# Kernel tuning notes

Hardware: AMD Instinct MI355X
Metric: run time of the kernel (lower is better)

The kernel has to match this reference:

```python
import jax, jax.numpy as jnp
import numpy as np

N_NODES = 50000
N_EDGES = 400000
HEADS = 4
OUT_CH = 128
IN_CH = 128
NEG_SLOPE = 0.2  # PyG GATConv default


def setup_inputs() -> dict:
    key = jax.random.key(0)
    ks = jax.random.split(key, 6)
    x = jax.random.normal(ks[0], (N_NODES, IN_CH), dtype=jnp.float32)
    edge_index = jax.random.randint(ks[1], (2, N_EDGES), 0, N_NODES, dtype=jnp.int64)
    # glorot-ish scaling for numerical sanity
    W = jax.random.normal(ks[2], (IN_CH, HEADS * OUT_CH), dtype=jnp.float32) * (1.0 / np.sqrt(IN_CH))
    att_src = jax.random.normal(ks[3], (1, HEADS, OUT_CH), dtype=jnp.float32) * (1.0 / np.sqrt(OUT_CH))
    att_dst = jax.random.normal(ks[4], (1, HEADS, OUT_CH), dtype=jnp.float32) * (1.0 / np.sqrt(OUT_CH))
    bias = jax.random.normal(ks[5], (HEADS * OUT_CH,), dtype=jnp.float32) * 0.01
    return {"x": x, "edge_index": edge_index, "W": W, "att_src": att_src, "att_dst": att_dst, "bias": bias}


def reference(x, edge_index, W, att_src, att_dst, bias):
    # PyG GATConv forward (eval mode -> attention dropout is identity), concat=True.
    N = x.shape[0]
    # add self loops (PyG default add_self_loops=True)
    loops = jnp.arange(N, dtype=edge_index.dtype)
    src = jnp.concatenate([edge_index[0], loops])  # message sources
    dst = jnp.concatenate([edge_index[1], loops])  # aggregation targets

    h = (x @ W).reshape(N, HEADS, OUT_CH)                 # [N,H,C]
    a_src = jnp.sum(h * att_src, axis=-1)                 # [N,H]
    a_dst = jnp.sum(h * att_dst, axis=-1)                 # [N,H]

    e = jax.nn.leaky_relu(a_src[src] + a_dst[dst], NEG_SLOPE)  # [E,H]
    # scatter-softmax over incoming edges of each dst node (every node has a self loop)
    e_max = jax.ops.segment_max(e, dst, num_segments=N)        # [N,H]
    e_exp = jnp.exp(e - e_max[dst])                            # [E,H]
    denom = jax.ops.segment_sum(e_exp, dst, num_segments=N)    # [N,H]
    alpha = e_exp / denom[dst]                                 # [E,H]

    msg = h[src] * alpha[:, :, None]                           # [E,H,C]
    out = jax.ops.segment_sum(msg, dst, num_segments=N)        # [N,H,C]
    return out.reshape(N, HEADS * OUT_CH) + bias
```

## Files before the change

### kernel.cpp

```cpp
#include <hip/hip_runtime.h>
#include <math.h>

#define N_NODES 50000
#define N_EDGES 400000
#define HEADS 4
#define CH 128
#define HC 512
#define NEG_SLOPE 0.2f
#define CAP 48

typedef float f32x4 __attribute__((ext_vector_type(4)));
typedef short bf16x8 __attribute__((ext_vector_type(8)));
typedef int   i32x4 __attribute__((ext_vector_type(4)));
typedef unsigned short u16x8 __attribute__((ext_vector_type(8)));

__device__ inline unsigned short f2bf(float f) {
    unsigned int u = __float_as_uint(f);
    unsigned int r = (u + 0x7FFFu + ((u >> 16) & 1u)) >> 16;
    return (unsigned short)r;
}
__device__ inline float bf2f(unsigned short u) {
    return __uint_as_float(((unsigned int)u) << 16);
}

#define CASTNB 256
#define ZNB    ((N_NODES + 255) / 256)
#define DEGNB  ((N_EDGES + 255) / 256)

__global__ __launch_bounds__(256) void k_prep(const float* __restrict__ W,
                                              unsigned short* __restrict__ Wsw,
                                              int* __restrict__ cnt) {
    const int bid = blockIdx.x, tid = threadIdx.x;
    if (bid < CASTNB) {
        int i = bid * 256 + tid;
        int k = i >> 9, n = i & 511;
        int kt = k >> 5, kk = k & 31;
        int nt = n >> 4, nn = n & 15;
        int lane = ((kk >> 3) << 4) | nn;
        int j = kk & 7;
        Wsw[((size_t)(kt * 32 + nt) * 64 + lane) * 8 + j] = f2bf(W[i]);
    } else {
        int i = (bid - CASTNB) * 256 + tid;
        if (i < N_NODES) cnt[i] = 0;
    }
}

__global__ __launch_bounds__(256) void k_fillslot(const int* __restrict__ ei,
                                                  int* __restrict__ cnt,
                                                  int* __restrict__ slot) {
    int e = blockIdx.x * 256 + threadIdx.x;
    if (e >= N_EDGES) return;
    int s = ei[e];
    int d = ei[N_EDGES + e];
    int pos = atomicAdd(&cnt[d], 1);
    if (pos < CAP) slot[d * CAP + pos] = s;
}

#define AP 136
#define OP 520
#define BM 16
#define GEMMNB (N_NODES / BM)

__global__ __launch_bounds__(256) void k_gemm(const float* __restrict__ x,
                                              const unsigned short* __restrict__ Wsw,
                                              const float* __restrict__ att_src,
                                              const float* __restrict__ att_dst,
                                              unsigned short* __restrict__ h,
                                              float* __restrict__ a_src,
                                              float* __restrict__ a_dst) {
    __shared__ unsigned short lds[BM * OP];

    const int r0  = blockIdx.x * BM;
    const int tid = threadIdx.x;

    {
        const f32x4* x4 = (const f32x4*)x;
#pragma unroll
        for (int i = 0; i < 2; ++i) {
            int idx = i * 256 + tid;
            int row = idx >> 5;
            int c4  = idx & 31;
            f32x4 v = __builtin_nontemporal_load(&x4[(size_t)(r0 + row) * 32 + c4]);
            ushort4 b;
            b.x = f2bf(v.x); b.y = f2bf(v.y); b.z = f2bf(v.z); b.w = f2bf(v.w);
            *(ushort4*)&lds[row * AP + c4 * 4] = b;
        }
    }
    __syncthreads();

    const int wave = tid >> 6;
    const int lane = tid & 63;
    const int mrow = lane & 15;
    const int kgrp = lane >> 4;
    const int ntg0 = wave * 8;

    f32x4 acc[8];
#pragma unroll
    for (int nt = 0; nt < 8; ++nt) acc[nt] = (f32x4)(0.f);

#pragma unroll
    for (int kt = 0; kt < 4; ++kt) {
        bf16x8 a0 = *(const bf16x8*)&lds[mrow * AP + kt * 32 + kgrp * 8];
#pragma unroll
        for (int nt = 0; nt < 8; ++nt) {
            bf16x8 b = *(const bf16x8*)&Wsw[((size_t)(kt * 32 + ntg0 + nt) * 64 + lane) * 8];
            acc[nt] = __builtin_amdgcn_mfma_f32_16x16x32_bf16(a0, b, acc[nt], 0, 0, 0);
        }
    }

    {
        float as[8], adv[8];
#pragma unroll
        for (int nt = 0; nt < 8; ++nt) {
            as[nt]  = att_src[wave * 128 + nt * 16 + mrow];
            adv[nt] = att_dst[wave * 128 + nt * 16 + mrow];
        }
#pragma unroll
        for (int r = 0; r < 4; ++r) {
            float sv = 0.f, dv = 0.f;
#pragma unroll
            for (int nt = 0; nt < 8; ++nt) {
                sv += acc[nt][r] * as[nt];
                dv += acc[nt][r] * adv[nt];
            }
#pragma unroll
            for (int off = 1; off < 16; off <<= 1) {
                sv += __shfl_xor(sv, off);
                dv += __shfl_xor(dv, off);
            }
            if (mrow == 0) {
                int grow = r0 + kgrp * 4 + r;
                a_src[grow * HEADS + wave] = sv;
                a_dst[grow * HEADS + wave] = dv;
            }
        }
    }

    __syncthreads();
#pragma unroll
    for (int nt = 0; nt < 8; ++nt)
#pragma unroll
        for (int r = 0; r < 4; ++r)
            lds[(kgrp * 4 + r) * OP + wave * 128 + nt * 16 + mrow] = f2bf(acc[nt][r]);
    __syncthreads();

#pragma unroll
    for (int i = 0; i < 4; ++i) {
        int idx = i * 256 + tid;
        int row = idx >> 6;
        int c   = idx & 63;
        ushort4 lo = *(ushort4*)&lds[row * OP + c * 8];
        ushort4 hi = *(ushort4*)&lds[row * OP + c * 8 + 4];
        *(ushort4*)&h[(size_t)(r0 + row) * HC + c * 8]     = lo;
        *(ushort4*)&h[(size_t)(r0 + row) * HC + c * 8 + 4] = hi;
    }
}

__global__ __launch_bounds__(64) void k_gather(const int* __restrict__ cnt,
                                               const int* __restrict__ slot,
                                               const unsigned short* __restrict__ h,
                                               const float* __restrict__ a_src,
                                               const float* __restrict__ a_dst,
                                               const float* __restrict__ bias,
                                               float* __restrict__ out) {
    const int n    = blockIdx.x;
    const int lane = threadIdx.x;
    const int head = lane >> 4;
    const int c0   = lane * 8;

    const float ad = a_dst[n * HEADS + head];

    float e0 = a_src[n * HEADS + head] + ad;
    e0 = e0 > 0.f ? e0 : NEG_SLOPE * e0;
    float ex = __expf(e0);
    u16x8 hv = *(const u16x8*)&h[(size_t)n * HC + c0];
    float acc[8];
#pragma unroll
    for (int j = 0; j < 8; ++j) acc[j] = ex * bf2f(hv[j]);
    float den = ex;

    int m = cnt[n];
    if (m > CAP) m = CAP;
    const int base = n * CAP;

    for (int i0 = 0; i0 < m; i0 += 8) {
        const int rem = m - i0;
        i32x4 sa = *(const i32x4*)&slot[base + i0];
        i32x4 sb = *(const i32x4*)&slot[base + i0 + 4];
        int s0 = (0 < rem) ? sa.x : n;
        int s1 = (1 < rem) ? sa.y : n;
        int s2 = (2 < rem) ? sa.z : n;
        int s3 = (3 < rem) ? sa.w : n;
        int s4 = (4 < rem) ? sb.x : n;
        int s5 = (5 < rem) ? sb.y : n;
        int s6 = (6 < rem) ? sb.z : n;
        int s7 = (7 < rem) ? sb.w : n;
        u16x8 v0 = *(const u16x8*)&h[(size_t)s0 * HC + c0];
        u16x8 v1 = *(const u16x8*)&h[(size_t)s1 * HC + c0];
        u16x8 v2 = *(const u16x8*)&h[(size_t)s2 * HC + c0];
        u16x8 v3 = *(const u16x8*)&h[(size_t)s3 * HC + c0];
        u16x8 v4 = *(const u16x8*)&h[(size_t)s4 * HC + c0];
        u16x8 v5 = *(const u16x8*)&h[(size_t)s5 * HC + c0];
        u16x8 v6 = *(const u16x8*)&h[(size_t)s6 * HC + c0];
        u16x8 v7 = *(const u16x8*)&h[(size_t)s7 * HC + c0];
        float f0 = a_src[s0 * HEADS + head] + ad;
        float f1 = a_src[s1 * HEADS + head] + ad;
        float f2 = a_src[s2 * HEADS + head] + ad;
        float f3 = a_src[s3 * HEADS + head] + ad;
        float f4 = a_src[s4 * HEADS + head] + ad;
        float f5 = a_src[s5 * HEADS + head] + ad;
        float f6 = a_src[s6 * HEADS + head] + ad;
        float f7 = a_src[s7 * HEADS + head] + ad;
        f0 = f0 > 0.f ? f0 : NEG_SLOPE * f0;
        f1 = f1 > 0.f ? f1 : NEG_SLOPE * f1;
        f2 = f2 > 0.f ? f2 : NEG_SLOPE * f2;
        f3 = f3 > 0.f ? f3 : NEG_SLOPE * f3;
        f4 = f4 > 0.f ? f4 : NEG_SLOPE * f4;
        f5 = f5 > 0.f ? f5 : NEG_SLOPE * f5;
        f6 = f6 > 0.f ? f6 : NEG_SLOPE * f6;
        f7 = f7 > 0.f ? f7 : NEG_SLOPE * f7;
        float w0 = (0 < rem) ? __expf(f0) : 0.f;
        float w1 = (1 < rem) ? __expf(f1) : 0.f;
        float w2 = (2 < rem) ? __expf(f2) : 0.f;
        float w3 = (3 < rem) ? __expf(f3) : 0.f;
        float w4 = (4 < rem) ? __expf(f4) : 0.f;
        float w5 = (5 < rem) ? __expf(f5) : 0.f;
        float w6 = (6 < rem) ? __expf(f6) : 0.f;
        float w7 = (7 < rem) ? __expf(f7) : 0.f;
#pragma unroll
        for (int j = 0; j < 8; ++j) {
            acc[j] += w0 * bf2f(v0[j]) + w1 * bf2f(v1[j])
                    + w2 * bf2f(v2[j]) + w3 * bf2f(v3[j]);
            acc[j] += w4 * bf2f(v4[j]) + w5 * bf2f(v5[j])
                    + w6 * bf2f(v6[j]) + w7 * bf2f(v7[j]);
        }
        den += ((w0 + w1) + (w2 + w3)) + ((w4 + w5) + (w6 + w7));
    }

    float inv = 1.f / den;
    f32x4 b0 = ((const f32x4*)bias)[lane * 2];
    f32x4 b1 = ((const f32x4*)bias)[lane * 2 + 1];
    f32x4 o0, o1;
    o0.x = acc[0] * inv + b0.x; o0.y = acc[1] * inv + b0.y;
    o0.z = acc[2] * inv + b0.z; o0.w = acc[3] * inv + b0.w;
    o1.x = acc[4] * inv + b1.x; o1.y = acc[5] * inv + b1.y;
    o1.z = acc[6] * inv + b1.z; o1.w = acc[7] * inv + b1.w;
    __builtin_nontemporal_store(o0, (f32x4*)out + (size_t)n * 128 + lane * 2);
    __builtin_nontemporal_store(o1, (f32x4*)out + (size_t)n * 128 + lane * 2 + 1);
}

extern "C" void kernel_launch(void* const* d_in, const int* in_sizes, int n_in,
                              void* d_out, int out_size, void* d_ws, size_t ws_size,
                              hipStream_t stream) {
    const float* x       = (const float*)d_in[0];
    const int*   ei      = (const int*)  d_in[1];
    const float* W       = (const float*)d_in[2];
    const float* att_src = (const float*)d_in[3];
    const float* att_dst = (const float*)d_in[4];
    const float* bias    = (const float*)d_in[5];
    float* out = (float*)d_out;

    unsigned short* h   = (unsigned short*)d_ws;
    unsigned short* Wsw = h + (size_t)N_NODES * HC;
    float* a_src = (float*)(Wsw + 128 * HC);
    float* a_dst = a_src + N_NODES * HEADS;
    int*   cnt   = (int*)(a_dst + N_NODES * HEADS);
    int*   slot  = cnt + N_NODES;

    k_prep    <<<CASTNB + ZNB, 256, 0, stream>>>(W, Wsw, cnt);
    k_fillslot<<<DEGNB, 256, 0, stream>>>(ei, cnt, slot);
    k_gemm    <<<GEMMNB, 256, 0, stream>>>(x, Wsw, att_src, att_dst, h, a_src, a_dst);
    k_gather  <<<N_NODES, 64, 0, stream>>>(cnt, slot, h, a_src, a_dst, bias, out);
}
```

Before: 260.9 us.

## Merge slot fill into GEMM launch and widen gather to 128 threads

The edge-slot fill kernel is folded into the GEMM launch as extra leading blocks, so the fill and the GEMM run concurrently in one launch and one kernel boundary goes away. The gather kernel now uses 128 threads per node with 4 channels each and unrolls by 4 edges instead of 8, which raises thread-level parallelism but issues more, narrower loads and performs fewer gathers per thread in flight. The fill blocks with early return do affect the GEMM block scheduling order.

```diff
diff --git a/kernel.cpp b/kernel.cpp
--- a/kernel.cpp
+++ b/kernel.cpp
@@ -12,7 +12,6 @@
 typedef float f32x4 __attribute__((ext_vector_type(4)));
 typedef short bf16x8 __attribute__((ext_vector_type(8)));
 typedef int   i32x4 __attribute__((ext_vector_type(4)));
-typedef unsigned short u16x8 __attribute__((ext_vector_type(8)));
 
 __device__ inline unsigned short f2bf(float f) {
     unsigned int u = __float_as_uint(f);
@@ -25,7 +24,7 @@
 
 #define CASTNB 256
 #define ZNB    ((N_NODES + 255) / 256)
-#define DEGNB  ((N_EDGES + 255) / 256)
+#define FILLNB ((N_EDGES + 255) / 256)
 
 __global__ __launch_bounds__(256) void k_prep(const float* __restrict__ W,
                                               unsigned short* __restrict__ Wsw,
@@ -45,17 +44,6 @@
     }
 }
 
-__global__ __launch_bounds__(256) void k_fillslot(const int* __restrict__ ei,
-                                                  int* __restrict__ cnt,
-                                                  int* __restrict__ slot) {
-    int e = blockIdx.x * 256 + threadIdx.x;
-    if (e >= N_EDGES) return;
-    int s = ei[e];
-    int d = ei[N_EDGES + e];
-    int pos = atomicAdd(&cnt[d], 1);
-    if (pos < CAP) slot[d * CAP + pos] = s;
-}
-
 #define AP 136
 #define OP 520
 #define BM 16
@@ -67,10 +55,24 @@
                                               const float* __restrict__ att_dst,
                                               unsigned short* __restrict__ h,
                                               float* __restrict__ a_src,
-                                              float* __restrict__ a_dst) {
+                                              float* __restrict__ a_dst,
+                                              const int* __restrict__ ei,
+                                              int* __restrict__ cnt,
+                                              int* __restrict__ slot) {
     __shared__ unsigned short lds[BM * OP];
 
-    const int r0  = blockIdx.x * BM;
+    if (blockIdx.x < FILLNB) {
+        int e = blockIdx.x * 256 + threadIdx.x;
+        if (e < N_EDGES) {
+            int s = ei[e];
+            int d = ei[N_EDGES + e];
+            int pos = atomicAdd(&cnt[d], 1);
+            if (pos < CAP) slot[d * CAP + pos] = s;
+        }
+        return;
+    }
+
+    const int r0  = (blockIdx.x - FILLNB) * BM;
     const int tid = threadIdx.x;
 
     {
@@ -156,97 +158,69 @@
     }
 }
 
-__global__ __launch_bounds__(64) void k_gather(const int* __restrict__ cnt,
-                                               const int* __restrict__ slot,
-                                               const unsigned short* __restrict__ h,
-                                               const float* __restrict__ a_src,
-                                               const float* __restrict__ a_dst,
-                                               const float* __restrict__ bias,
-                                               float* __restrict__ out) {
+__global__ __launch_bounds__(128) void k_gather(const int* __restrict__ cnt,
+                                                const int* __restrict__ slot,
+                                                const unsigned short* __restrict__ h,
+                                                const float* __restrict__ a_src,
+                                                const float* __restrict__ a_dst,
+                                                const float* __restrict__ bias,
+                                                float* __restrict__ out) {
     const int n    = blockIdx.x;
-    const int lane = threadIdx.x;
-    const int head = lane >> 4;
-    const int c0   = lane * 8;
+    const int t    = threadIdx.x;
+    const int head = t >> 5;
+    const int c0   = t * 4;
 
     const float ad = a_dst[n * HEADS + head];
 
     float e0 = a_src[n * HEADS + head] + ad;
     e0 = e0 > 0.f ? e0 : NEG_SLOPE * e0;
     float ex = __expf(e0);
-    u16x8 hv = *(const u16x8*)&h[(size_t)n * HC + c0];
-    float acc[8];
-#pragma unroll
-    for (int j = 0; j < 8; ++j) acc[j] = ex * bf2f(hv[j]);
+    ushort4 hv = *(const ushort4*)&h[(size_t)n * HC + c0];
+    float4 acc;
+    acc.x = ex * bf2f(hv.x); acc.y = ex * bf2f(hv.y);
+    acc.z = ex * bf2f(hv.z); acc.w = ex * bf2f(hv.w);
     float den = ex;
 
     int m = cnt[n];
     if (m > CAP) m = CAP;
     const int base = n * CAP;
 
-    for (int i0 = 0; i0 < m; i0 += 8) {
+    for (int i0 = 0; i0 < m; i0 += 4) {
         const int rem = m - i0;
-        i32x4 sa = *(const i32x4*)&slot[base + i0];
-        i32x4 sb = *(const i32x4*)&slot[base + i0 + 4];
-        int s0 = (0 < rem) ? sa.x : n;
-        int s1 = (1 < rem) ? sa.y : n;
-        int s2 = (2 < rem) ? sa.z : n;
-        int s3 = (3 < rem) ? sa.w : n;
-        int s4 = (4 < rem) ? sb.x : n;
-        int s5 = (5 < rem) ? sb.y : n;
-        int s6 = (6 < rem) ? sb.z : n;
-        int s7 = (7 < rem) ? sb.w : n;
-        u16x8 v0 = *(const u16x8*)&h[(size_t)s0 * HC + c0];
-        u16x8 v1 = *(const u16x8*)&h[(size_t)s1 * HC + c0];
-        u16x8 v2 = *(const u16x8*)&h[(size_t)s2 * HC + c0];
-        u16x8 v3 = *(const u16x8*)&h[(size_t)s3 * HC + c0];
-        u16x8 v4 = *(const u16x8*)&h[(size_t)s4 * HC + c0];
-        u16x8 v5 = *(const u16x8*)&h[(size_t)s5 * HC + c0];
-        u16x8 v6 = *(const u16x8*)&h[(size_t)s6 * HC + c0];
-        u16x8 v7 = *(const u16x8*)&h[(size_t)s7 * HC + c0];
+        i32x4 s4 = *(const i32x4*)&slot[base + i0];
+        int s0 = (0 < rem) ? s4.x : n;
+        int s1 = (1 < rem) ? s4.y : n;
+        int s2 = (2 < rem) ? s4.z : n;
+        int s3 = (3 < rem) ? s4.w : n;
         float f0 = a_src[s0 * HEADS + head] + ad;
         float f1 = a_src[s1 * HEADS + head] + ad;
         float f2 = a_src[s2 * HEADS + head] + ad;
         float f3 = a_src[s3 * HEADS + head] + ad;
-        float f4 = a_src[s4 * HEADS + head] + ad;
-        float f5 = a_src[s5 * HEADS + head] + ad;
-        float f6 = a_src[s6 * HEADS + head] + ad;
-        float f7 = a_src[s7 * HEADS + head] + ad;
+        ushort4 v0 = *(const ushort4*)&h[(size_t)s0 * HC + c0];
+        ushort4 v1 = *(const ushort4*)&h[(size_t)s1 * HC + c0];
+        ushort4 v2 = *(const ushort4*)&h[(size_t)s2 * HC + c0];
+        ushort4 v3 = *(const ushort4*)&h[(size_t)s3 * HC + c0];
         f0 = f0 > 0.f ? f0 : NEG_SLOPE * f0;
         f1 = f1 > 0.f ? f1 : NEG_SLOPE * f1;
         f2 = f2 > 0.f ? f2 : NEG_SLOPE * f2;
         f3 = f3 > 0.f ? f3 : NEG_SLOPE * f3;
-        f4 = f4 > 0.f ? f4 : NEG_SLOPE * f4;
-        f5 = f5 > 0.f ? f5 : NEG_SLOPE * f5;
-        f6 = f6 > 0.f ? f6 : NEG_SLOPE * f6;
-        f7 = f7 > 0.f ? f7 : NEG_SLOPE * f7;
         float w0 = (0 < rem) ? __expf(f0) : 0.f;
         float w1 = (1 < rem) ? __expf(f1) : 0.f;
         float w2 = (2 < rem) ? __expf(f2) : 0.f;
         float w3 = (3 < rem) ? __expf(f3) : 0.f;
-        float w4 = (4 < rem) ? __expf(f4) : 0.f;
-        float w5 = (5 < rem) ? __expf(f5) : 0.f;
-        float w6 = (6 < rem) ? __expf(f6) : 0.f;
-        float w7 = (7 < rem) ? __expf(f7) : 0.f;
-#pragma unroll
-        for (int j = 0; j < 8; ++j) {
-            acc[j] += w0 * bf2f(v0[j]) + w1 * bf2f(v1[j])
-                    + w2 * bf2f(v2[j]) + w3 * bf2f(v3[j]);
-            acc[j] += w4 * bf2f(v4[j]) + w5 * bf2f(v5[j])
-                    + w6 * bf2f(v6[j]) + w7 * bf2f(v7[j]);
-        }
-        den += ((w0 + w1) + (w2 + w3)) + ((w4 + w5) + (w6 + w7));
+        acc.x += w0 * bf2f(v0.x) + w1 * bf2f(v1.x) + w2 * bf2f(v2.x) + w3 * bf2f(v3.x);
+        acc.y += w0 * bf2f(v0.y) + w1 * bf2f(v1.y) + w2 * bf2f(v2.y) + w3 * bf2f(v3.y);
+        acc.z += w0 * bf2f(v0.z) + w1 * bf2f(v1.z) + w2 * bf2f(v2.z) + w3 * bf2f(v3.z);
+        acc.w += w0 * bf2f(v0.w) + w1 * bf2f(v1.w) + w2 * bf2f(v2.w) + w3 * bf2f(v3.w);
+        den += (w0 + w1) + (w2 + w3);
     }
 
     float inv = 1.f / den;
-    f32x4 b0 = ((const f32x4*)bias)[lane * 2];
-    f32x4 b1 = ((const f32x4*)bias)[lane * 2 + 1];
-    f32x4 o0, o1;
-    o0.x = acc[0] * inv + b0.x; o0.y = acc[1] * inv + b0.y;
-    o0.z = acc[2] * inv + b0.z; o0.w = acc[3] * inv + b0.w;
-    o1.x = acc[4] * inv + b1.x; o1.y = acc[5] * inv + b1.y;
-    o1.z = acc[6] * inv + b1.z; o1.w = acc[7] * inv + b1.w;
-    __builtin_nontemporal_store(o0, (f32x4*)out + (size_t)n * 128 + lane * 2);
-    __builtin_nontemporal_store(o1, (f32x4*)out + (size_t)n * 128 + lane * 2 + 1);
+    float4 b = ((const float4*)bias)[t];
+    f32x4 o;
+    o.x = acc.x * inv + b.x; o.y = acc.y * inv + b.y;
+    o.z = acc.z * inv + b.z; o.w = acc.w * inv + b.w;
+    __builtin_nontemporal_store(o, (f32x4*)out + (size_t)n * 128 + t);
 }
 
 extern "C" void kernel_launch(void* const* d_in, const int* in_sizes, int n_in,
@@ -267,8 +241,8 @@
     int*   cnt   = (int*)(a_dst + N_NODES * HEADS);
     int*   slot  = cnt + N_NODES;
 
-    k_prep    <<<CASTNB + ZNB, 256, 0, stream>>>(W, Wsw, cnt);
-    k_fillslot<<<DEGNB, 256, 0, stream>>>(ei, cnt, slot);
-    k_gemm    <<<GEMMNB, 256, 0, stream>>>(x, Wsw, att_src, att_dst, h, a_src, a_dst);
-    k_gather  <<<N_NODES, 64, 0, stream>>>(cnt, slot, h, a_src, a_dst, bias, out);
-}
+    k_prep  <<<CASTNB + ZNB, 256, 0, stream>>>(W, Wsw, cnt);
+    k_gemm  <<<FILLNB + GEMMNB, 256, 0, stream>>>(x, Wsw, att_src, att_dst, h,
+                                                  a_src, a_dst, ei, cnt, slot);
+    k_gather<<<N_NODES, 128, 0, stream>>>(cnt, slot, h, a_src, a_dst, bias, out);
+}
```

After: 242.3 us. 7.1% less time.
